# Kernel optimization log

Measured on AMD Instinct MI355X. Metric: run time of the kernel, lower is better.

Reference implementation:

```python
import jax, jax.numpy as jnp
import numpy as np

# init hyperparameters (from init_kwargs)
KD = KH = KW = 3
SD = SH = SW = 1
PD = PH = PW = 1
DD = DH = DW = 1
GROUPS = 1
DG = 1  # deformable_groups
CIN, COUT = 32, 64


def setup_inputs() -> dict:
    key = jax.random.key(0)
    k1, k2, k3, k4, k5 = jax.random.split(key, 5)
    B, D, H, W = 2, 8, 48, 48
    K = KD * KH * KW
    x = jax.random.normal(k1, (B, CIN, D, H, W), dtype=jnp.float32)
    # 2 offset components (h, w) per deformable-group kernel tap
    offset = jax.random.normal(k2, (B, 2 * DG * K, D, H, W), dtype=jnp.float32)
    mask = jax.random.uniform(k3, (B, DG * K, D, H, W), dtype=jnp.float32)
    fan_in = CIN // GROUPS * K
    weight = jax.random.normal(k4, (COUT, CIN // GROUPS, KD, KH, KW), dtype=jnp.float32) / np.sqrt(fan_in)
    bias = jax.random.uniform(k5, (COUT,), dtype=jnp.float32, minval=-1.0, maxval=1.0) / np.sqrt(fan_in)
    return {"input": x, "offset": offset, "mask": mask, "weight": weight, "bias": bias}


def reference(input, offset, mask, weight, bias):
    x = input
    B, Cin, D, H, W = x.shape
    Cout = weight.shape[0]
    K = KD * KH * KW
    Do = (D + 2 * PD - DD * (KD - 1) - 1) // SD + 1
    Ho = (H + 2 * PH - DH * (KH - 1) - 1) // SH + 1
    Wo = (W + 2 * PW - DW * (KW - 1) - 1) // SW + 1
    Cg = Cin // DG

    kdi, khi, kwi = [a.reshape(-1) for a in jnp.meshgrid(
        jnp.arange(KD), jnp.arange(KH), jnp.arange(KW), indexing="ij")]
    # depth taps: regular (un-deformed) dilated grid -> exact integer index
    d_pos = kdi[:, None] * DD + jnp.arange(Do) * SD - PD           # [K, Do]
    valid_d = (d_pos >= 0) & (d_pos < D)
    d_idx = jnp.clip(d_pos, 0, D - 1)
    h_base = (khi[:, None] * DH + jnp.arange(Ho) * SH - PH).astype(x.dtype)  # [K, Ho]
    w_base = (kwi[:, None] * DW + jnp.arange(Wo) * SW - PW).astype(x.dtype)  # [K, Wo]

    off = offset.reshape(B, DG, K, 2, Do, Ho, Wo)
    m = mask.reshape(B, DG, K, Do, Ho, Wo)

    h = h_base[None, None, :, None, :, None] + off[:, :, :, 0]     # [B,DG,K,Do,Ho,Wo]
    w = w_base[None, None, :, None, None, :] + off[:, :, :, 1]
    h0f, w0f = jnp.floor(h), jnp.floor(w)
    lh, lw = h - h0f, w - w0f
    h0, w0 = h0f.astype(jnp.int32), w0f.astype(jnp.int32)
    h1, w1 = h0 + 1, w0 + 1

    vd = valid_d[None, None, :, :, None, None]
    inb_h = lambda hi: (hi >= 0) & (hi < H)
    inb_w = lambda wi: (wi >= 0) & (wi < W)

    xg = x.reshape(B, DG, Cg, D, H, W)

    def gather(hI, wI):
        hc = jnp.clip(hI, 0, H - 1)
        wc = jnp.clip(wI, 0, W - 1)
        def per(xi, hh, ww):  # xi [Cg,D,H,W]; hh,ww [K,Do,Ho,Wo]
            dfull = jnp.broadcast_to(d_idx[:, :, None, None], hh.shape)
            return xi[:, dfull, hh, ww]  # [Cg,K,Do,Ho,Wo]
        return jax.vmap(jax.vmap(per))(xg, hc, wc)  # [B,DG,Cg,K,Do,Ho,Wo]

    w00 = ((1 - lh) * (1 - lw) * (inb_h(h0) & inb_w(w0) & vd))[:, :, None]
    w01 = ((1 - lh) * lw * (inb_h(h0) & inb_w(w1) & vd))[:, :, None]
    w10 = (lh * (1 - lw) * (inb_h(h1) & inb_w(w0) & vd))[:, :, None]
    w11 = (lh * lw * (inb_h(h1) & inb_w(w1) & vd))[:, :, None]

    val = (gather(h0, w0) * w00 + gather(h0, w1) * w01 +
           gather(h1, w0) * w10 + gather(h1, w1) * w11)   # [B,DG,Cg,K,Do,Ho,Wo]

    sampled = (val * m[:, :, None]).reshape(B, Cin, K, Do, Ho, Wo)
    w2 = weight.reshape(Cout, Cin // GROUPS, K)  # groups == 1
    out = jnp.einsum("bckdhw,ock->bodhw", sampled, w2)
    return out + bias[None, :, None, None, None]
```

## Files before the change

kernel.cpp:

```cpp
#include <hip/hip_runtime.h>
#include <hip/hip_fp16.h>

#define BSZ 2
#define CIN 32
#define COUT 64
#define DD_ 8
#define HH_ 48
#define WW_ 48
#define KK 27
#define HWs (HH_*WW_)
#define DHW (DD_*HH_*WW_)
#define NBLK (BSZ*DD_*HH_)
#define NT 768

typedef __attribute__((ext_vector_type(8))) _Float16 half8;
typedef __attribute__((ext_vector_type(4))) float f32x4;

__device__ __forceinline__ half8 splat_h(unsigned packed, int hi) {
    union { unsigned v; _Float16 h[2]; } c; c.v = packed;
    _Float16 e = c.h[hi];
    return (half8){e, e, e, e, e, e, e, e};
}

__device__ __forceinline__ void wg_barrier() {
    asm volatile("s_waitcnt lgkmcnt(0)" ::: "memory");
    __builtin_amdgcn_s_barrier();
    asm volatile("" ::: "memory");
}

__global__ void prep(const float* __restrict__ x, const float* __restrict__ wsrc,
                     _Float16* __restrict__ xT, _Float16* __restrict__ wf) {
    __shared__ float tile[CIN][WW_];
    int blk = blockIdx.x;
    if (blk < NBLK) {
        int h = blk % HH_;
        int t0 = blk / HH_;
        int d = t0 % DD_;
        int b = t0 / DD_;
        int base = d * HWs + h * WW_;
        for (int e = threadIdx.x; e < CIN * WW_; e += 256) {
            int ci = e / WW_, w = e - ci * WW_;
            tile[ci][w] = x[(size_t)(b * CIN + ci) * DHW + base + w];
        }
        __syncthreads();
        for (int e = threadIdx.x; e < CIN * WW_; e += 256) {
            int w = e >> 5, ci = e & 31;
            xT[(size_t)(b * DHW + base + w) * CIN + ci] = (_Float16)tile[ci][w];
        }
    } else {
        int idx = (blk - NBLK) * 256 + threadIdx.x;
        if (idx < KK * 4 * 64 * 8) {
            int j = idx & 7, l = (idx >> 3) & 63, c = (idx >> 9) & 3, k = idx >> 11;
            int co = c * 16 + (l & 15), ci = (l >> 4) * 8 + j;
            wf[idx] = (_Float16)wsrc[(co * CIN + ci) * KK + k];
        }
    }
}

template<int USE_XT>
__launch_bounds__(NT, 6)
__global__ void dcn3d(const float* __restrict__ x, const _Float16* __restrict__ xT,
                      const float* __restrict__ off, const float* __restrict__ msk,
                      const float* __restrict__ wsrc, const _Float16* __restrict__ wf,
                      const float* __restrict__ bias, float* __restrict__ out) {
    int blk = blockIdx.x;
    int h = blk % HH_;
    int t0 = blk / HH_;
    int d = t0 % DD_;
    int b = t0 / DD_;

    __shared__ uint4 Pp[KK * WW_];
    __shared__ half8 Sh[3][4 * 3 * 64];

    int tid = threadIdx.x;
    int lane = tid & 63;
    int wid = tid >> 6;
    int cstrip = wid & 3;
    int T = wid >> 2;
    int spb = d * HWs + h * WW_;

    const _Float16* xTb = xT + (size_t)b * DHW * CIN;
    const float* xb = x + (size_t)b * CIN * DHW;

    for (int p = tid; p < KK * WW_; p += NT) {
        int k = p / WW_;
        int w = p - k * WW_;
        int kd = k / 9, kh2 = (k / 3) % 3, kw2 = k % 3;
        int dpos = d + kd - 1;
        bool vd = (dpos >= 0) && (dpos < DD_);
        int didx = min(max(dpos, 0), DD_ - 1);
        int rb = didx * HWs;
        int sp = spb + w;
        float oh = off[(b * (2 * KK) + 2 * k) * DHW + sp];
        float ow = off[(b * (2 * KK) + 2 * k + 1) * DHW + sp];
        float m  = msk[(b * KK + k) * DHW + sp];
        float vm = vd ? m : 0.f;
        float hhf = (float)(kh2 + h - 1) + oh;
        float wwf = (float)(kw2 + w - 1) + ow;
        float h0f = floorf(hhf), w0f = floorf(wwf);
        float lh = hhf - h0f, lw = wwf - w0f;
        int h0 = (int)h0f, w0 = (int)w0f, h1 = h0 + 1, w1 = w0 + 1;
        bool ih0 = (h0 >= 0) && (h0 < HH_), ih1 = (h1 >= 0) && (h1 < HH_);
        bool iw0 = (w0 >= 0) && (w0 < WW_), iw1 = (w1 >= 0) && (w1 < WW_);
        int h0c = min(max(h0, 0), HH_ - 1), h1c = min(max(h1, 0), HH_ - 1);
        int w0c = min(max(w0, 0), WW_ - 1), w1c = min(max(w1, 0), WW_ - 1);
        float f00 = (ih0 && iw0) ? (1.f - lh) * (1.f - lw) * vm : 0.f;
        float f01 = (ih0 && iw1) ? (1.f - lh) * lw * vm : 0.f;
        float f10 = (ih1 && iw0) ? lh * (1.f - lw) * vm : 0.f;
        float f11 = (ih1 && iw1) ? lh * lw * vm : 0.f;
        uint4 P;
        P.x = (unsigned)(rb + h0c * WW_ + w0c) | ((unsigned)(rb + h0c * WW_ + w1c) << 16);
        P.y = (unsigned)(rb + h1c * WW_ + w0c) | ((unsigned)(rb + h1c * WW_ + w1c) << 16);
        __half2 ha = __floats2half2_rn(f00, f01);
        __half2 hb = __floats2half2_rn(f10, f11);
        P.z = *(const unsigned*)&ha;
        P.w = *(const unsigned*)&hb;
        Pp[p] = P;
    }
    wg_barrier();

    half8 qA00 = {}, qA01 = {}, qA10 = {}, qA11 = {};
    half8 qB00 = {}, qB01 = {}, qB10 = {}, qB11 = {};
    unsigned wzA = 0, wwA = 0, wzB = 0, wwB = 0;
    int sbA = 0, sbB = 0;

#define ISSUE(S, KB, NKg)                                                        \
    if ((NKg) == 4 || tid < (NKg) * 192) {                                       \
        int p = tid >> 2, g = tid & 3;                                           \
        int kl = p / WW_, w = p - kl * WW_;                                      \
        uint4 P = Pp[((KB) + kl) * WW_ + w];                                     \
        wz##S = P.z; ww##S = P.w;                                                \
        sb##S = (kl * 3 + (w >> 4)) * 64 + g * 16 + (w & 15);                    \
        if (USE_XT) {                                                            \
            const _Float16* bp = xTb + g * 8;                                    \
            q##S##00 = *(const half8*)(bp + ((size_t)(P.x & 0xFFFFu) << 5));     \
            q##S##01 = *(const half8*)(bp + ((size_t)(P.x >> 16) << 5));         \
            q##S##10 = *(const half8*)(bp + ((size_t)(P.y & 0xFFFFu) << 5));     \
            q##S##11 = *(const half8*)(bp + ((size_t)(P.y >> 16) << 5));         \
        } else {                                                                 \
            _Pragma("unroll")                                                    \
            for (int j = 0; j < 8; ++j) {                                        \
                const float* xp = xb + (size_t)(g * 8 + j) * DHW;                \
                q##S##00[j] = (_Float16)xp[P.x & 0xFFFFu];                       \
                q##S##01[j] = (_Float16)xp[P.x >> 16];                           \
                q##S##10[j] = (_Float16)xp[P.y & 0xFFFFu];                       \
                q##S##11[j] = (_Float16)xp[P.y >> 16];                           \
            }                                                                    \
        }                                                                        \
    }

#define WRITE(S, BUF, NKg)                                                       \
    if ((NKg) == 4 || tid < (NKg) * 192)                                         \
        Sh[BUF][sb##S] = q##S##00 * splat_h(wz##S, 0) + q##S##01 * splat_h(wz##S, 1) \
                       + q##S##10 * splat_h(ww##S, 0) + q##S##11 * splat_h(ww##S, 1);

    f32x4 acc = {0.f, 0.f, 0.f, 0.f};

#define GEMM(NKg, KB, BUF)                                                       \
    _Pragma("unroll")                                                            \
    for (int kl = 0; kl < (NKg); ++kl) {                                         \
        half8 a;                                                                 \
        if (USE_XT) {                                                            \
            a = *(const half8*)(wf + ((((KB) + kl) * 4 + cstrip) * 64 + lane) * 8); \
        } else {                                                                 \
            int co = cstrip * 16 + (lane & 15);                                  \
            int ci0 = (lane >> 4) * 8;                                           \
            _Pragma("unroll")                                                    \
            for (int j = 0; j < 8; ++j)                                          \
                a[j] = (_Float16)wsrc[(co * CIN + ci0 + j) * KK + (KB) + kl];    \
        }                                                                        \
        half8 bfr = Sh[BUF][(kl * 3 + T) * 64 + (lane >> 4) * 16 + (lane & 15)]; \
        acc = __builtin_amdgcn_mfma_f32_16x16x32_f16(a, bfr, acc, 0, 0, 0);      \
    }

    ISSUE(A, 0, 4)
    ISSUE(B, 4, 4)
    WRITE(A, 0, 4)
    wg_barrier();

    ISSUE(A, 8, 4)
    GEMM(4, 0, 0)
    WRITE(B, 1, 4)
    wg_barrier();

    ISSUE(B, 12, 4)
    GEMM(4, 4, 1)
    WRITE(A, 2, 4)
    wg_barrier();

    ISSUE(A, 16, 4)
    GEMM(4, 8, 2)
    WRITE(B, 0, 4)
    wg_barrier();

    ISSUE(B, 20, 4)
    GEMM(4, 12, 0)
    WRITE(A, 1, 4)
    wg_barrier();

    ISSUE(A, 24, 3)
    GEMM(4, 16, 1)
    WRITE(B, 2, 4)
    wg_barrier();

    GEMM(4, 20, 2)
    WRITE(A, 0, 3)
    wg_barrier();

    GEMM(3, 24, 0)

#undef ISSUE
#undef WRITE
#undef GEMM

    int co0 = cstrip * 16 + (lane >> 4) * 4;
    int wcol = T * 16 + (lane & 15);
#pragma unroll
    for (int r = 0; r < 4; ++r)
        out[((b * COUT + co0 + r) * DD_ + d) * HWs + h * WW_ + wcol] = acc[r] + bias[co0 + r];
}

extern "C" void kernel_launch(void* const* d_in, const int* in_sizes, int n_in,
                              void* d_out, int out_size, void* d_ws, size_t ws_size,
                              hipStream_t stream) {
    const float* x    = (const float*)d_in[0];
    const float* off  = (const float*)d_in[1];
    const float* msk  = (const float*)d_in[2];
    const float* w    = (const float*)d_in[3];
    const float* bias = (const float*)d_in[4];
    float* out = (float*)d_out;

    const size_t XT_OFF   = 131072;
    const size_t XT_BYTES = (size_t)BSZ * DHW * CIN * sizeof(_Float16);

    _Float16* wf = (_Float16*)d_ws;
    _Float16* xT = (_Float16*)((char*)d_ws + XT_OFF);
    int use = (ws_size >= XT_OFF + XT_BYTES) ? 1 : 0;

    if (use) {
        int wblocks = (KK * 4 * 64 * 8 + 255) / 256;
        prep<<<NBLK + wblocks, 256, 0, stream>>>(x, w, xT, wf);
        dcn3d<1><<<NBLK, NT, 0, stream>>>(x, xT, off, msk, w, wf, bias, out);
    } else {
        dcn3d<0><<<NBLK, NT, 0, stream>>>(x, xT, off, msk, w, wf, bias, out);
    }
}
```

Baseline: 35.64 us.

## Split each output row into three 16-column blocks of 256 threads

The fused deformable conv kernel now launches three times as many blocks, each covering 16 output columns with 4 waves instead of a 768-thread block covering all 48 columns. Shared memory per block shrinks (sampling params for 16 columns, double-buffered B tiles instead of triple), which should raise occupancy and spread work across more CUs. The cost is that each block recomputes its own slice of the parameters and reloads the weight fragments, and pipelining depth drops from triple to double buffering. The fallback path without a workspace is replaced by a simple scalar reference kernel.

```diff
diff --git a/kernel.cpp b/kernel.cpp
--- a/kernel.cpp
+++ b/kernel.cpp
@@ -11,7 +11,7 @@
 #define HWs (HH_*WW_)
 #define DHW (DD_*HH_*WW_)
 #define NBLK (BSZ*DD_*HH_)
-#define NT 768
+#define NTH 256
 
 typedef __attribute__((ext_vector_type(8))) _Float16 half8;
 typedef __attribute__((ext_vector_type(4))) float f32x4;
@@ -57,167 +57,195 @@
     }
 }
 
-template<int USE_XT>
-__launch_bounds__(NT, 6)
-__global__ void dcn3d(const float* __restrict__ x, const _Float16* __restrict__ xT,
+__launch_bounds__(NTH, 4)
+__global__ void dcn3d(const _Float16* __restrict__ xT,
                       const float* __restrict__ off, const float* __restrict__ msk,
-                      const float* __restrict__ wsrc, const _Float16* __restrict__ wf,
+                      const _Float16* __restrict__ wf,
                       const float* __restrict__ bias, float* __restrict__ out) {
+    int blk = blockIdx.x;
+    int T = blk % 3;
+    int row = blk / 3;
+    int h = row % HH_;
+    int t0 = row / HH_;
+    int d = t0 % DD_;
+    int b = t0 / DD_;
+    int T16 = T * 16;
+
+    __shared__ uint4 Pp[KK * 16];
+    __shared__ half8 Sh[2][4 * 64];
+
+    int tid = threadIdx.x;
+    int lane = tid & 63;
+    int q = tid >> 6;
+    int spb = d * HWs + h * WW_;
+
+#define PARAM(PIDX)                                                            \
+    {                                                                          \
+        int p = (PIDX);                                                        \
+        int k = p >> 4;                                                        \
+        int wl_ = p & 15;                                                      \
+        int w = T16 + wl_;                                                     \
+        int kd = k / 9, kh2 = (k / 3) % 3, kw2 = k % 3;                        \
+        int dpos = d + kd - 1;                                                 \
+        bool vd = (dpos >= 0) && (dpos < DD_);                                 \
+        int didx = min(max(dpos, 0), DD_ - 1);                                 \
+        int rb = didx * HWs;                                                   \
+        int sp = spb + w;                                                      \
+        float oh = off[(b * (2 * KK) + 2 * k) * DHW + sp];                     \
+        float ow = off[(b * (2 * KK) + 2 * k + 1) * DHW + sp];                 \
+        float m  = msk[(b * KK + k) * DHW + sp];                               \
+        float vm = vd ? m : 0.f;                                               \
+        float hhf = (float)(kh2 + h - 1) + oh;                                 \
+        float wwf = (float)(kw2 + w - 1) + ow;                                 \
+        float h0f = floorf(hhf), w0f = floorf(wwf);                            \
+        float lh = hhf - h0f, lw = wwf - w0f;                                  \
+        int h0 = (int)h0f, w0 = (int)w0f, h1 = h0 + 1, w1 = w0 + 1;            \
+        bool ih0 = (h0 >= 0) && (h0 < HH_), ih1 = (h1 >= 0) && (h1 < HH_);     \
+        bool iw0 = (w0 >= 0) && (w0 < WW_), iw1 = (w1 >= 0) && (w1 < WW_);     \
+        int h0c = min(max(h0, 0), HH_ - 1), h1c = min(max(h1, 0), HH_ - 1);    \
+        int w0c = min(max(w0, 0), WW_ - 1), w1c = min(max(w1, 0), WW_ - 1);    \
+        float f00 = (ih0 && iw0) ? (1.f - lh) * (1.f - lw) * vm : 0.f;         \
+        float f01 = (ih0 && iw1) ? (1.f - lh) * lw * vm : 0.f;                 \
+        float f10 = (ih1 && iw0) ? lh * (1.f - lw) * vm : 0.f;                 \
+        float f11 = (ih1 && iw1) ? lh * lw * vm : 0.f;                         \
+        uint4 P;                                                               \
+        P.x = (unsigned)(rb + h0c * WW_ + w0c)                                 \
+            | ((unsigned)(rb + h0c * WW_ + w1c) << 16);                        \
+        P.y = (unsigned)(rb + h1c * WW_ + w0c)                                 \
+            | ((unsigned)(rb + h1c * WW_ + w1c) << 16);                        \
+        __half2 ha = __floats2half2_rn(f00, f01);                              \
+        __half2 hb = __floats2half2_rn(f10, f11);                              \
+        P.z = *(const unsigned*)&ha;                                           \
+        P.w = *(const unsigned*)&hb;                                           \
+        Pp[p] = P;                                                             \
+    }
+
+    PARAM(tid)
+    if (tid < KK * 16 - NTH) PARAM(tid + NTH)
+#undef PARAM
+    wg_barrier();
+
+    const _Float16* bp = xT + (size_t)b * DHW * CIN + ((tid >> 4) & 3) * 8;
+
+    half8 qA00 = {}, qA01 = {}, qA10 = {}, qA11 = {};
+    half8 qB00 = {}, qB01 = {}, qB10 = {}, qB11 = {};
+    unsigned wzA = 0, wwA = 0, wzB = 0, wwB = 0;
+
+#define ISSUE(S, KB, NKg)                                                        \
+    if ((NKg) == 4 || tid < (NKg) * 64) {                                        \
+        int kl = tid >> 6;                                                       \
+        uint4 P = Pp[((KB) + kl) * 16 + (tid & 15)];                             \
+        wz##S = P.z; ww##S = P.w;                                                \
+        q##S##00 = *(const half8*)(bp + ((size_t)(P.x & 0xFFFFu) << 5));         \
+        q##S##01 = *(const half8*)(bp + ((size_t)(P.x >> 16) << 5));             \
+        q##S##10 = *(const half8*)(bp + ((size_t)(P.y & 0xFFFFu) << 5));         \
+        q##S##11 = *(const half8*)(bp + ((size_t)(P.y >> 16) << 5));             \
+    }
+
+#define WRITE(S, BUF, NKg)                                                       \
+    if ((NKg) == 4 || tid < (NKg) * 64)                                          \
+        Sh[BUF][tid] = q##S##00 * splat_h(wz##S, 0) + q##S##01 * splat_h(wz##S, 1)\
+                     + q##S##10 * splat_h(ww##S, 0) + q##S##11 * splat_h(ww##S, 1);
+
+    f32x4 acc = {0.f, 0.f, 0.f, 0.f};
+
+#define GEMM(NKg, KB, BUF)                                                       \
+    _Pragma("unroll")                                                            \
+    for (int kl = 0; kl < (NKg); ++kl) {                                         \
+        half8 a = *(const half8*)(wf + ((((KB) + kl) * 4 + q) * 64 + lane) * 8); \
+        half8 bfr = Sh[BUF][kl * 64 + lane];                                     \
+        acc = __builtin_amdgcn_mfma_f32_16x16x32_f16(a, bfr, acc, 0, 0, 0);      \
+    }
+
+    ISSUE(A, 0, 4)
+    WRITE(A, 0, 4)
+    wg_barrier();
+
+    ISSUE(B, 4, 4)
+    GEMM(4, 0, 0)
+    WRITE(B, 1, 4)
+    wg_barrier();
+
+    ISSUE(A, 8, 4)
+    GEMM(4, 4, 1)
+    WRITE(A, 0, 4)
+    wg_barrier();
+
+    ISSUE(B, 12, 4)
+    GEMM(4, 8, 0)
+    WRITE(B, 1, 4)
+    wg_barrier();
+
+    ISSUE(A, 16, 4)
+    GEMM(4, 12, 1)
+    WRITE(A, 0, 4)
+    wg_barrier();
+
+    ISSUE(B, 20, 4)
+    GEMM(4, 16, 0)
+    WRITE(B, 1, 4)
+    wg_barrier();
+
+    ISSUE(A, 24, 3)
+    GEMM(4, 20, 1)
+    WRITE(A, 0, 3)
+    wg_barrier();
+
+    GEMM(3, 24, 0)
+
+#undef ISSUE
+#undef WRITE
+#undef GEMM
+
+    int co0 = q * 16 + (lane >> 4) * 4;
+    int wcol = T16 + (lane & 15);
+#pragma unroll
+    for (int r = 0; r < 4; ++r)
+        out[((b * COUT + co0 + r) * DD_ + d) * HWs + h * WW_ + wcol] = acc[r] + bias[co0 + r];
+}
+
+__global__ void dcn3d_ref(const float* __restrict__ x, const float* __restrict__ off,
+                          const float* __restrict__ msk, const float* __restrict__ w,
+                          const float* __restrict__ bias, float* __restrict__ out) {
     int blk = blockIdx.x;
     int h = blk % HH_;
     int t0 = blk / HH_;
     int d = t0 % DD_;
     int b = t0 / DD_;
-
-    __shared__ uint4 Pp[KK * WW_];
-    __shared__ half8 Sh[3][4 * 3 * 64];
-
-    int tid = threadIdx.x;
-    int lane = tid & 63;
-    int wid = tid >> 6;
-    int cstrip = wid & 3;
-    int T = wid >> 2;
-    int spb = d * HWs + h * WW_;
-
-    const _Float16* xTb = xT + (size_t)b * DHW * CIN;
-    const float* xb = x + (size_t)b * CIN * DHW;
-
-    for (int p = tid; p < KK * WW_; p += NT) {
-        int k = p / WW_;
-        int w = p - k * WW_;
-        int kd = k / 9, kh2 = (k / 3) % 3, kw2 = k % 3;
-        int dpos = d + kd - 1;
-        bool vd = (dpos >= 0) && (dpos < DD_);
-        int didx = min(max(dpos, 0), DD_ - 1);
-        int rb = didx * HWs;
-        int sp = spb + w;
-        float oh = off[(b * (2 * KK) + 2 * k) * DHW + sp];
-        float ow = off[(b * (2 * KK) + 2 * k + 1) * DHW + sp];
-        float m  = msk[(b * KK + k) * DHW + sp];
-        float vm = vd ? m : 0.f;
-        float hhf = (float)(kh2 + h - 1) + oh;
-        float wwf = (float)(kw2 + w - 1) + ow;
-        float h0f = floorf(hhf), w0f = floorf(wwf);
-        float lh = hhf - h0f, lw = wwf - w0f;
-        int h0 = (int)h0f, w0 = (int)w0f, h1 = h0 + 1, w1 = w0 + 1;
-        bool ih0 = (h0 >= 0) && (h0 < HH_), ih1 = (h1 >= 0) && (h1 < HH_);
-        bool iw0 = (w0 >= 0) && (w0 < WW_), iw1 = (w1 >= 0) && (w1 < WW_);
-        int h0c = min(max(h0, 0), HH_ - 1), h1c = min(max(h1, 0), HH_ - 1);
-        int w0c = min(max(w0, 0), WW_ - 1), w1c = min(max(w1, 0), WW_ - 1);
-        float f00 = (ih0 && iw0) ? (1.f - lh) * (1.f - lw) * vm : 0.f;
-        float f01 = (ih0 && iw1) ? (1.f - lh) * lw * vm : 0.f;
-        float f10 = (ih1 && iw0) ? lh * (1.f - lw) * vm : 0.f;
-        float f11 = (ih1 && iw1) ? lh * lw * vm : 0.f;
-        uint4 P;
-        P.x = (unsigned)(rb + h0c * WW_ + w0c) | ((unsigned)(rb + h0c * WW_ + w1c) << 16);
-        P.y = (unsigned)(rb + h1c * WW_ + w0c) | ((unsigned)(rb + h1c * WW_ + w1c) << 16);
-        __half2 ha = __floats2half2_rn(f00, f01);
-        __half2 hb = __floats2half2_rn(f10, f11);
-        P.z = *(const unsigned*)&ha;
-        P.w = *(const unsigned*)&hb;
-        Pp[p] = P;
-    }
-    wg_barrier();
-
-    half8 qA00 = {}, qA01 = {}, qA10 = {}, qA11 = {};
-    half8 qB00 = {}, qB01 = {}, qB10 = {}, qB11 = {};
-    unsigned wzA = 0, wwA = 0, wzB = 0, wwB = 0;
-    int sbA = 0, sbB = 0;
-
-#define ISSUE(S, KB, NKg)                                                        \
-    if ((NKg) == 4 || tid < (NKg) * 192) {                                       \
-        int p = tid >> 2, g = tid & 3;                                           \
-        int kl = p / WW_, w = p - kl * WW_;                                      \
-        uint4 P = Pp[((KB) + kl) * WW_ + w];                                     \
-        wz##S = P.z; ww##S = P.w;                                                \
-        sb##S = (kl * 3 + (w >> 4)) * 64 + g * 16 + (w & 15);                    \
-        if (USE_XT) {                                                            \
-            const _Float16* bp = xTb + g * 8;                                    \
-            q##S##00 = *(const half8*)(bp + ((size_t)(P.x & 0xFFFFu) << 5));     \
-            q##S##01 = *(const half8*)(bp + ((size_t)(P.x >> 16) << 5));         \
-            q##S##10 = *(const half8*)(bp + ((size_t)(P.y & 0xFFFFu) << 5));     \
-            q##S##11 = *(const half8*)(bp + ((size_t)(P.y >> 16) << 5));         \
-        } else {                                                                 \
-            _Pragma("unroll")                                                    \
-            for (int j = 0; j < 8; ++j) {                                        \
-                const float* xp = xb + (size_t)(g * 8 + j) * DHW;                \
-                q##S##00[j] = (_Float16)xp[P.x & 0xFFFFu];                       \
-                q##S##01[j] = (_Float16)xp[P.x >> 16];                           \
-                q##S##10[j] = (_Float16)xp[P.y & 0xFFFFu];                       \
-                q##S##11[j] = (_Float16)xp[P.y >> 16];                           \
-            }                                                                    \
-        }                                                                        \
-    }
-
-#define WRITE(S, BUF, NKg)                                                       \
-    if ((NKg) == 4 || tid < (NKg) * 192)                                         \
-        Sh[BUF][sb##S] = q##S##00 * splat_h(wz##S, 0) + q##S##01 * splat_h(wz##S, 1) \
-                       + q##S##10 * splat_h(ww##S, 0) + q##S##11 * splat_h(ww##S, 1);
-
-    f32x4 acc = {0.f, 0.f, 0.f, 0.f};
-
-#define GEMM(NKg, KB, BUF)                                                       \
-    _Pragma("unroll")                                                            \
-    for (int kl = 0; kl < (NKg); ++kl) {                                         \
-        half8 a;                                                                 \
-        if (USE_XT) {                                                            \
-            a = *(const half8*)(wf + ((((KB) + kl) * 4 + cstrip) * 64 + lane) * 8); \
-        } else {                                                                 \
-            int co = cstrip * 16 + (lane & 15);                                  \
-            int ci0 = (lane >> 4) * 8;                                           \
-            _Pragma("unroll")                                                    \
-            for (int j = 0; j < 8; ++j)                                          \
-                a[j] = (_Float16)wsrc[(co * CIN + ci0 + j) * KK + (KB) + kl];    \
-        }                                                                        \
-        half8 bfr = Sh[BUF][(kl * 3 + T) * 64 + (lane >> 4) * 16 + (lane & 15)]; \
-        acc = __builtin_amdgcn_mfma_f32_16x16x32_f16(a, bfr, acc, 0, 0, 0);      \
-    }
-
-    ISSUE(A, 0, 4)
-    ISSUE(B, 4, 4)
-    WRITE(A, 0, 4)
-    wg_barrier();
-
-    ISSUE(A, 8, 4)
-    GEMM(4, 0, 0)
-    WRITE(B, 1, 4)
-    wg_barrier();
-
-    ISSUE(B, 12, 4)
-    GEMM(4, 4, 1)
-    WRITE(A, 2, 4)
-    wg_barrier();
-
-    ISSUE(A, 16, 4)
-    GEMM(4, 8, 2)
-    WRITE(B, 0, 4)
-    wg_barrier();
-
-    ISSUE(B, 20, 4)
-    GEMM(4, 12, 0)
-    WRITE(A, 1, 4)
-    wg_barrier();
-
-    ISSUE(A, 24, 3)
-    GEMM(4, 16, 1)
-    WRITE(B, 2, 4)
-    wg_barrier();
-
-    GEMM(4, 20, 2)
-    WRITE(A, 0, 3)
-    wg_barrier();
-
-    GEMM(3, 24, 0)
-
-#undef ISSUE
-#undef WRITE
-#undef GEMM
-
-    int co0 = cstrip * 16 + (lane >> 4) * 4;
-    int wcol = T * 16 + (lane & 15);
-#pragma unroll
-    for (int r = 0; r < 4; ++r)
-        out[((b * COUT + co0 + r) * DD_ + d) * HWs + h * WW_ + wcol] = acc[r] + bias[co0 + r];
+    for (int e = threadIdx.x; e < COUT * WW_; e += 256) {
+        int co = e / WW_, wo = e - co * WW_;
+        float acc = bias[co];
+        for (int k = 0; k < KK; ++k) {
+            int kd = k / 9, kh2 = (k / 3) % 3, kw2 = k % 3;
+            int dpos = d + kd - 1;
+            if (dpos < 0 || dpos >= DD_) continue;
+            int sp = d * HWs + h * WW_ + wo;
+            float oh = off[(b * (2 * KK) + 2 * k) * DHW + sp];
+            float ow = off[(b * (2 * KK) + 2 * k + 1) * DHW + sp];
+            float m  = msk[(b * KK + k) * DHW + sp];
+            float hhf = (float)(kh2 + h - 1) + oh;
+            float wwf = (float)(kw2 + wo - 1) + ow;
+            float h0f = floorf(hhf), w0f = floorf(wwf);
+            float lh = hhf - h0f, lw = wwf - w0f;
+            int h0 = (int)h0f, w0 = (int)w0f, h1 = h0 + 1, w1 = w0 + 1;
+            bool ih0 = (h0 >= 0) && (h0 < HH_), ih1 = (h1 >= 0) && (h1 < HH_);
+            bool iw0 = (w0 >= 0) && (w0 < WW_), iw1 = (w1 >= 0) && (w1 < WW_);
+            int h0c = min(max(h0, 0), HH_ - 1), h1c = min(max(h1, 0), HH_ - 1);
+            int w0c = min(max(w0, 0), WW_ - 1), w1c = min(max(w1, 0), WW_ - 1);
+            float f00 = (ih0 && iw0) ? (1.f - lh) * (1.f - lw) * m : 0.f;
+            float f01 = (ih0 && iw1) ? (1.f - lh) * lw * m : 0.f;
+            float f10 = (ih1 && iw0) ? lh * (1.f - lw) * m : 0.f;
+            float f11 = (ih1 && iw1) ? lh * lw * m : 0.f;
+            int rb = dpos * HWs;
+            for (int ci = 0; ci < CIN; ++ci) {
+                const float* xp = x + (size_t)(b * CIN + ci) * DHW;
+                float v = f00 * xp[rb + h0c * WW_ + w0c] + f01 * xp[rb + h0c * WW_ + w1c]
+                        + f10 * xp[rb + h1c * WW_ + w0c] + f11 * xp[rb + h1c * WW_ + w1c];
+                acc += w[(co * CIN + ci) * KK + k] * v;
+            }
+        }
+        out[((b * COUT + co) * DD_ + d) * HWs + h * WW_ + wo] = acc;
+    }
 }
 
 extern "C" void kernel_launch(void* const* d_in, const int* in_sizes, int n_in,
@@ -240,8 +268,8 @@
     if (use) {
         int wblocks = (KK * 4 * 64 * 8 + 255) / 256;
         prep<<<NBLK + wblocks, 256, 0, stream>>>(x, w, xT, wf);
-        dcn3d<1><<<NBLK, NT, 0, stream>>>(x, xT, off, msk, w, wf, bias, out);
+        dcn3d<<<NBLK * 3, NTH, 0, stream>>>(xT, off, msk, wf, bias, out);
     } else {
-        dcn3d<0><<<NBLK, NT, 0, stream>>>(x, xT, off, msk, w, wf, bias, out);
-    }
-}
+        dcn3d_ref<<<NBLK, 256, 0, stream>>>(x, off, msk, w, bias, out);
+    }
+}
```

Result: slower. 42.55 us (+19.4%).
